# Kernel tuning notes

Hardware: AMD Instinct MI355X
Metric: run time of the kernel (lower is better)

The kernel has to match this reference:

```python
import jax, jax.numpy as jnp
import numpy as np

N_NODES = 50000
N_EDGES = 1600000
LORA_R = 8


def gcn_conv(h, W, b, src, dst, n):
    # PyG GCNConv: linear transform, add self-loops, symmetric normalization,
    # scatter-add aggregation at target nodes, then bias.
    h = h @ W  # [N, out]
    ones = jnp.ones(src.shape[0], dtype=h.dtype)
    deg = jax.ops.segment_sum(ones, dst, num_segments=n) + 1.0  # +1 for self-loop
    dis = jax.lax.rsqrt(deg)  # deg >= 1 always
    norm = dis[src] * dis[dst]  # [E]
    agg = jax.ops.segment_sum(norm[:, None] * h[src], dst, num_segments=n)
    agg = agg + (dis * dis)[:, None] * h  # self-loop contribution
    return agg + b


def lora(h, A, B):
    # LoRALinear: b(a(x)) * (1/r); replaces input (not additive)
    return (h @ A) @ B * (1.0 / LORA_R)


def setup_inputs() -> dict:
    key = jax.random.key(0)
    ks = jax.random.split(key, 12)
    inp = {}
    inp['x'] = jax.random.normal(ks[0], (N_NODES, 128), dtype=jnp.float32)
    inp['edge_index'] = jax.random.randint(ks[1], (2, N_EDGES), 0, N_NODES, dtype=jnp.int64 if jax.config.jax_enable_x64 else jnp.int32)
    inp['domain_idx'] = jax.random.randint(ks[2], (N_NODES,), 0, 3, dtype=jnp.int32)
    inp['emb_table'] = jax.random.normal(ks[3], (3, 4096), dtype=jnp.float32)
    s1 = 1.0 / np.sqrt(4224.0)
    inp['W1'] = jax.random.normal(ks[4], (4224, 32), dtype=jnp.float32) * s1
    inp['b1'] = jnp.zeros((32,), dtype=jnp.float32)
    inp['A1'] = jax.random.normal(ks[5], (32, LORA_R), dtype=jnp.float32) * (1.0 / np.sqrt(32.0))
    inp['B1'] = jax.random.normal(ks[6], (LORA_R, 32), dtype=jnp.float32) * (1.0 / np.sqrt(LORA_R))
    inp['W2'] = jax.random.normal(ks[7], (32, 5), dtype=jnp.float32) * (1.0 / np.sqrt(32.0))
    inp['b2'] = jnp.zeros((5,), dtype=jnp.float32)
    inp['A2'] = jax.random.normal(ks[8], (5, LORA_R), dtype=jnp.float32) * (1.0 / np.sqrt(5.0))
    inp['B2'] = jax.random.normal(ks[9], (LORA_R, 5), dtype=jnp.float32) * (1.0 / np.sqrt(LORA_R))
    return inp


def reference(x, edge_index, domain_idx, emb_table, W1, b1, A1, B1, W2, b2, A2, B2):
    n = x.shape[0]
    src, dst = edge_index[0], edge_index[1]
    embedded = emb_table[domain_idx]  # [N, 4096]
    h = jnp.concatenate([embedded, x], axis=1)  # [N, 4224]
    h = gcn_conv(h, W1, b1, src, dst, n)
    h = lora(h, A1, B1)
    h = jax.nn.relu(h)
    h = gcn_conv(h, W2, b2, src, dst, n)
    h = lora(h, A2, B2)
    return jax.nn.log_softmax(h, axis=1)
```

## Files before the change

### kernel.cpp

```cpp
#include <hip/hip_runtime.h>
#include <hip/hip_bf16.h>
#include <hip/hip_fp16.h>


#define XDIM 128
#define EMBDIM 4096
#define TB 8192
#define BSH 6
#define BN 64
#define ECAP2 2560
#define MAXT 256

__global__ void __launch_bounds__(512) kA(
    const int* __restrict__ src, const int* __restrict__ dst,
    unsigned int* __restrict__ tedges, unsigned int* __restrict__ toffcnt,
    int e, int ntiles,
    const float* __restrict__ emb, const float* __restrict__ W1,
    float* __restrict__ emb_part,
    const float* __restrict__ A1, const float* __restrict__ A2,
    const float* __restrict__ B2, const float* __restrict__ b1,
    float* __restrict__ M2, float* __restrict__ b1A1,
    float* __restrict__ WA, int n) {
    __shared__ __align__(16) char smem[40960];
    int t = threadIdx.x, bx = blockIdx.x;
    if (bx < ntiles) {
        unsigned int* staged = (unsigned int*)smem;
        int* loff = (int*)(smem + 32768);
        int* rctr = (int*)(smem + 36864);
        int base = bx * TB;
        int len = min(TB, e - base);
        for (int i = t; i < 1024; i += 512) { loff[i] = 0; rctr[i] = 0; }
        __syncthreads();
        int sreg[16], dreg[16];
        #pragma unroll
        for (int k = 0; k < 16; ++k) {
            int i = t + k * 512;
            if (i < len) {
                sreg[k] = src[base + i];
                dreg[k] = dst[base + i];
            }
        }
        #pragma unroll
        for (int k = 0; k < 16; ++k) {
            int i = t + k * 512;
            if (i < len) atomicAdd(&loff[dreg[k] >> BSH], 1);
        }
        __syncthreads();
        if (t < 64) {
            int ch = t * 16;
            int v[16]; int s0 = 0;
            #pragma unroll
            for (int k = 0; k < 16; ++k) { v[k] = loff[ch + k]; s0 += v[k]; }
            int pre = s0;
            #pragma unroll
            for (int d2 = 1; d2 < 64; d2 <<= 1) {
                int up = __shfl_up(pre, d2);
                if (t >= d2) pre += up;
            }
            int excl = pre - s0;
            unsigned int* ocp = toffcnt + (size_t)bx * 1024 + ch;
            #pragma unroll
            for (int k = 0; k < 16; ++k) {
                loff[ch + k] = excl;
                ocp[k] = ((unsigned int)excl << 16) | (unsigned int)v[k];
                excl += v[k];
            }
        }
        __syncthreads();
        #pragma unroll
        for (int k = 0; k < 16; ++k) {
            int i = t + k * 512;
            if (i < len) {
                int b = dreg[k] >> BSH;
                int r = atomicAdd(&rctr[b], 1);
                staged[loff[b] + r] = ((unsigned int)dreg[k] << 16) | (unsigned int)sreg[k];
            }
        }
        __syncthreads();
        uint4* tw = (uint4*)(tedges + (size_t)bx * TB);
        const uint4* sr = (const uint4*)staged;
        int lw = (len + 3) >> 2;
        for (int i = t; i < lw; i += 512) tw[i] = sr[i];
    } else if (bx < ntiles + 96) {
        float* red = (float*)smem;
        int bx2 = bx - ntiles;
        int dm = bx2 >> 5, seg = bx2 & 31;
        const float* er = emb + dm * EMBDIM + seg * 128;
        const float* wr = W1 + (size_t)(seg * 128) * 32;
        int j = t & 31, kk = t >> 5;
        if (t < 256) {
            float acc = 0.f;
            for (int k2 = kk; k2 < 128; k2 += 8) acc += er[k2] * wr[k2 * 32 + j];
            red[kk * 32 + j] = acc;
        }
        __syncthreads();
        if (t < 32) {
            float s = 0.f;
            #pragma unroll
            for (int r = 0; r < 8; ++r) s += red[r * 32 + t];
            emb_part[bx2 * 32 + t] = s;
        }
        if (bx2 == 0) {
            if (t < 25) {
                int c = t / 5, cp = t % 5;
                float s = 0.f;
                #pragma unroll
                for (int r = 0; r < 8; ++r) s += A2[c * 8 + r] * B2[r * 5 + cp];
                M2[c * 5 + cp] = s * 0.125f;
            }
            if (t >= 32 && t < 40) {
                int j2 = t - 32;
                float s = 0.f;
                #pragma unroll
                for (int k = 0; k < 32; ++k) s += b1[k] * A1[k * 8 + j2];
                b1A1[j2] = s;
            }
        }
    } else {
        float* sA1 = (float*)smem;
        if (t < 256) sA1[t] = A1[t];
        __syncthreads();
        for (int idx = t; idx < 1024; idx += 512) {
            int k = idx >> 3, j = idx & 7;
            const float* wr = W1 + (size_t)(EMBDIM + k) * 32;
            float s = 0.f;
            #pragma unroll 8
            for (int c = 0; c < 32; ++c) s += wr[c] * sA1[c * 8 + j];
            WA[idx] = s;
        }
    }
}

__global__ void __launch_bounds__(256) kB(
    const unsigned int* __restrict__ tedges, const unsigned int* __restrict__ toffcnt,
    int ntiles,
    const float* __restrict__ emb_part, const float* __restrict__ A1,
    const int* __restrict__ dom, const float* __restrict__ x,
    const float* __restrict__ WA,
    int* __restrict__ deg, __half* __restrict__ p1h,
    unsigned short* __restrict__ nsrc, unsigned int* __restrict__ bm, int n) {
    __shared__ int hist[64], eoff[64], rctr[64], sdom[64];
    __shared__ int wtot[4];
    __shared__ unsigned short rbase[MAXT], soff[MAXT], slen[MAXT];
    __shared__ float sA1[256], sWA[1024], sproj[96], sembA1[24];
    __shared__ __align__(16) unsigned int ebuf[ECAP2];
    __shared__ __align__(16) unsigned short esrc[ECAP2];
    int t = threadIdx.x, b = blockIdx.x;
    int row0 = b << BSH;
    if (t < 64) {
        hist[t] = 0; rctr[t] = 0;
        int gi = row0 + t;
        sdom[t] = (gi < n) ? dom[gi] : 0;
    }
    sA1[t] = A1[t];
    #pragma unroll
    for (int q = 0; q < 4; ++q) sWA[t + q * 256] = WA[t + q * 256];
    if (t < 96) {
        int dm = t >> 5, c = t & 31;
        float s = 0.f;
        #pragma unroll
        for (int seg = 0; seg < 32; ++seg) s += emb_part[(dm * 32 + seg) * 32 + c];
        sproj[dm * 32 + c] = s;
    }
    {
        int w = t >> 6, l = t & 63;
        int i0 = w * 128 + l, i1 = w * 128 + 64 + l;
        unsigned int oc0 = (i0 < ntiles) ? toffcnt[(size_t)i0 * 1024 + b] : 0u;
        unsigned int oc1 = (i1 < ntiles) ? toffcnt[(size_t)i1 * 1024 + b] : 0u;
        int l0 = (int)(oc0 & 0xffffu), l1 = (int)(oc1 & 0xffffu);
        int p0 = l0, p1 = l1;
        #pragma unroll
        for (int d2 = 1; d2 < 64; d2 <<= 1) {
            int u0 = __shfl_up(p0, d2);
            int u1 = __shfl_up(p1, d2);
            if (l >= d2) { p0 += u0; p1 += u1; }
        }
        int totA = __shfl(p0, 63);
        if (l == 63) wtot[w] = p0 + p1;
        __syncthreads();
        int woff = 0;
        #pragma unroll
        for (int q = 0; q < 4; ++q) woff += (q < w) ? wtot[q] : 0;
        if (i0 < ntiles) {
            rbase[i0] = (unsigned short)min(woff + p0 - l0, 65535);
            soff[i0]  = (unsigned short)(oc0 >> 16);
            slen[i0]  = (unsigned short)l0;
        }
        if (i1 < ntiles) {
            rbase[i1] = (unsigned short)min(woff + totA + p1 - l1, 65535);
            soff[i1]  = (unsigned short)(oc1 >> 16);
            slen[i1]  = (unsigned short)l1;
        }
        if (t == 0) wtot[0] = wtot[0] + wtot[1] + wtot[2] + wtot[3];
    }
    __syncthreads();
    int m = wtot[0];
    if (m > ECAP2) m = ECAP2;
    if (t == 0) bm[b] = (unsigned int)m;
    {
        int g4 = t >> 2, l4 = t & 3;
        for (int tl = g4; tl < ntiles; tl += 64) {
            int l = slen[tl];
            if (l > 0) {
                const unsigned int* rp = tedges + (size_t)tl * TB + soff[tl];
                int bse = rbase[tl];
                for (int j = l4; j < l; j += 4) {
                    int p = bse + j;
                    if (p < ECAP2) ebuf[p] = rp[j];
                }
            }
        }
    }
    __syncthreads();
    for (int i = t; i < m; i += 256) atomicAdd(&hist[(ebuf[i] >> 16) & (BN - 1)], 1);
    __syncthreads();
    if (t < 64) {
        int v = hist[t];
        int pre = v;
        #pragma unroll
        for (int d2 = 1; d2 < 64; d2 <<= 1) {
            int up = __shfl_up(pre, d2);
            if (t >= d2) pre += up;
        }
        eoff[t] = pre - v;
        int gi = row0 + t;
        if (gi < n) deg[gi] = v;
    } else if (t < 88) {
        int dm = (t - 64) >> 3, j = (t - 64) & 7;
        float s = 0.f;
        #pragma unroll 8
        for (int c = 0; c < 32; ++c) s += sproj[dm * 32 + c] * sA1[c * 8 + j];
        sembA1[dm * 8 + j] = s;
    }
    __syncthreads();
    for (int i = t; i < m; i += 256) {
        unsigned int u = ebuf[i];
        int dl = (int)(u >> 16) & (BN - 1);
        int r = atomicAdd(&rctr[dl], 1);
        esrc[eoff[dl] + r] = (unsigned short)(u & 0xffffu);
    }
    for (int i = t; i < 512; i += 256) {
        int row = i >> 3, j = i & 7;
        int gi = row0 + row;
        if (gi < n) {
            const float4* xr = (const float4*)x + (size_t)gi * 32;
            float acc = 0.f;
            #pragma unroll 8
            for (int c4 = 0; c4 < 32; ++c4) {
                float4 v = xr[c4];
                acc += v.x * sWA[(c4 * 4 + 0) * 8 + j]
                     + v.y * sWA[(c4 * 4 + 1) * 8 + j]
                     + v.z * sWA[(c4 * 4 + 2) * 8 + j]
                     + v.w * sWA[(c4 * 4 + 3) * 8 + j];
            }
            float dd = rsqrtf((float)(hist[row] + 1));
            float val = acc + sembA1[sdom[row] * 8 + j];
            p1h[(size_t)gi * 8 + j] = __float2half_rn(dd * val);
        }
    }
    __syncthreads();
    {
        uint4* npw = (uint4*)(nsrc + (size_t)b * ECAP2);
        const uint4* ew = (const uint4*)esrc;
        int mw = (m + 7) >> 3;
        for (int i = t; i < mw; i += 256) npw[i] = ew[i];
    }
}

__global__ void __launch_bounds__(256) k_bagg1(
    const __half* __restrict__ p1h, const unsigned short* __restrict__ nsrc,
    const unsigned int* __restrict__ bm, const int* __restrict__ deg,
    const float* __restrict__ b1A1, const float* __restrict__ B1,
    const float* __restrict__ W2, __half* __restrict__ qh, int n) {
    __shared__ __align__(16) unsigned short esrc[ECAP2];
    __shared__ int eoff[BN], sdeg[BN];
    __shared__ float pacc[3][BN][8];
    __shared__ float sB1[256], sW2[160], sb[8];
    int t = threadIdx.x, b = blockIdx.x;
    int node0 = b << BSH;
    sB1[t] = B1[t];
    if (t < 160) sW2[t] = W2[t];
    if (t < 8) sb[t] = b1A1[t];
    if (t < 64) {
        int node = node0 + t;
        int v = (node < n) ? deg[node] : 0;
        sdeg[t] = v;
        int pre = v;
        #pragma unroll
        for (int d2 = 1; d2 < 64; d2 <<= 1) {
            int up = __shfl_up(pre, d2);
            if (t >= d2) pre += up;
        }
        eoff[t] = pre - v;
    }
    __syncthreads();
    int m = (int)bm[b];
    if (m > ECAP2) m = ECAP2;
    {
        const uint4* npw = (const uint4*)(nsrc + (size_t)b * ECAP2);
        uint4* ew = (uint4*)esrc;
        int mw = (m + 7) >> 3;
        for (int i = t; i < mw; i += 256) ew[i] = npw[i];
    }
    __syncthreads();
    int nodeL = t & (BN - 1), tsub = t >> BSH;
    int base0 = eoff[nodeL], c = sdeg[nodeL];
    float a[8] = {0,0,0,0,0,0,0,0}, a2[8] = {0,0,0,0,0,0,0,0};
    float a3[8] = {0,0,0,0,0,0,0,0}, a4[8] = {0,0,0,0,0,0,0,0};
    int k = tsub;
    for (; k + 12 < c; k += 16) {
        int s1 = esrc[base0 + k],     s2 = esrc[base0 + k + 4];
        int s3 = esrc[base0 + k + 8], s4 = esrc[base0 + k + 12];
        uint4 u = *(const uint4*)(p1h + (size_t)s1 * 8);
        uint4 v = *(const uint4*)(p1h + (size_t)s2 * 8);
        uint4 w = *(const uint4*)(p1h + (size_t)s3 * 8);
        uint4 y = *(const uint4*)(p1h + (size_t)s4 * 8);
        float2 f;
        f = __half22float2(*(__half2*)&u.x); a[0] += f.x; a[1] += f.y;
        f = __half22float2(*(__half2*)&u.y); a[2] += f.x; a[3] += f.y;
        f = __half22float2(*(__half2*)&u.z); a[4] += f.x; a[5] += f.y;
        f = __half22float2(*(__half2*)&u.w); a[6] += f.x; a[7] += f.y;
        f = __half22float2(*(__half2*)&v.x); a2[0] += f.x; a2[1] += f.y;
        f = __half22float2(*(__half2*)&v.y); a2[2] += f.x; a2[3] += f.y;
        f = __half22float2(*(__half2*)&v.z); a2[4] += f.x; a2[5] += f.y;
        f = __half22float2(*(__half2*)&v.w); a2[6] += f.x; a2[7] += f.y;
        f = __half22float2(*(__half2*)&w.x); a3[0] += f.x; a3[1] += f.y;
        f = __half22float2(*(__half2*)&w.y); a3[2] += f.x; a3[3] += f.y;
        f = __half22float2(*(__half2*)&w.z); a3[4] += f.x; a3[5] += f.y;
        f = __half22float2(*(__half2*)&w.w); a3[6] += f.x; a3[7] += f.y;
        f = __half22float2(*(__half2*)&y.x); a4[0] += f.x; a4[1] += f.y;
        f = __half22float2(*(__half2*)&y.y); a4[2] += f.x; a4[3] += f.y;
        f = __half22float2(*(__half2*)&y.z); a4[4] += f.x; a4[5] += f.y;
        f = __half22float2(*(__half2*)&y.w); a4[6] += f.x; a4[7] += f.y;
    }
    for (; k + 4 < c; k += 8) {
        int s1 = esrc[base0 + k], s2 = esrc[base0 + k + 4];
        uint4 u = *(const uint4*)(p1h + (size_t)s1 * 8);
        uint4 v = *(const uint4*)(p1h + (size_t)s2 * 8);
        float2 f;
        f = __half22float2(*(__half2*)&u.x); a[0] += f.x; a[1] += f.y;
        f = __half22float2(*(__half2*)&u.y); a[2] += f.x; a[3] += f.y;
        f = __half22float2(*(__half2*)&u.z); a[4] += f.x; a[5] += f.y;
        f = __half22float2(*(__half2*)&u.w); a[6] += f.x; a[7] += f.y;
        f = __half22float2(*(__half2*)&v.x); a2[0] += f.x; a2[1] += f.y;
        f = __half22float2(*(__half2*)&v.y); a2[2] += f.x; a2[3] += f.y;
        f = __half22float2(*(__half2*)&v.z); a2[4] += f.x; a2[5] += f.y;
        f = __half22float2(*(__half2*)&v.w); a2[6] += f.x; a2[7] += f.y;
    }
    for (; k < c; k += 4) {
        int s1 = esrc[base0 + k];
        uint4 u = *(const uint4*)(p1h + (size_t)s1 * 8);
        float2 f;
        f = __half22float2(*(__half2*)&u.x); a[0] += f.x; a[1] += f.y;
        f = __half22float2(*(__half2*)&u.y); a[2] += f.x; a[3] += f.y;
        f = __half22float2(*(__half2*)&u.z); a[4] += f.x; a[5] += f.y;
        f = __half22float2(*(__half2*)&u.w); a[6] += f.x; a[7] += f.y;
    }
    #pragma unroll
    for (int j = 0; j < 8; ++j) a[j] += a2[j] + a3[j] + a4[j];
    if (tsub > 0) {
        #pragma unroll
        for (int j = 0; j < 8; ++j) pacc[tsub - 1][nodeL][j] = a[j];
    }
    __syncthreads();
    if (t < BN) {
        int node = node0 + t;
        if (node < n) {
            float dd = rsqrtf((float)(sdeg[t] + 1));
            uint4 u = *(const uint4*)(p1h + (size_t)node * 8);
            float2 f;
            float af[8];
            f = __half22float2(*(__half2*)&u.x); af[0] = a[0] + f.x; af[1] = a[1] + f.y;
            f = __half22float2(*(__half2*)&u.y); af[2] = a[2] + f.x; af[3] = a[3] + f.y;
            f = __half22float2(*(__half2*)&u.z); af[4] = a[4] + f.x; af[5] = a[5] + f.y;
            f = __half22float2(*(__half2*)&u.w); af[6] = a[6] + f.x; af[7] = a[7] + f.y;
            #pragma unroll
            for (int ps = 0; ps < 3; ++ps) {
                #pragma unroll
                for (int j = 0; j < 8; ++j) af[j] += pacc[ps][t][j];
            }
            #pragma unroll
            for (int j = 0; j < 8; ++j) af[j] = dd * af[j] + sb[j];
            float qv[5] = {0.f, 0.f, 0.f, 0.f, 0.f};
            #pragma unroll
            for (int c2 = 0; c2 < 32; ++c2) {
                float tv = 0.f;
                #pragma unroll
                for (int j = 0; j < 8; ++j) tv += af[j] * sB1[j * 32 + c2];
                float st = fmaxf(tv * 0.125f, 0.f);
                #pragma unroll
                for (int o = 0; o < 5; ++o) qv[o] += st * sW2[c2 * 5 + o];
            }
            #pragma unroll
            for (int o = 0; o < 5; ++o) qh[(size_t)node * 8 + o] = __float2half_rn(dd * qv[o]);
        }
    }
}

__global__ void __launch_bounds__(256) k_bagg2(
    const __half* __restrict__ qh, const unsigned short* __restrict__ nsrc,
    const unsigned int* __restrict__ bm, const int* __restrict__ deg,
    const float* __restrict__ b2, const float* __restrict__ M2,
    float* __restrict__ out, int n) {
    __shared__ __align__(16) unsigned short esrc[ECAP2];
    __shared__ int eoff[BN], sdeg[BN];
    __shared__ float pacc[3][BN][5];
    __shared__ float sM2[25], sb2[5];
    int t = threadIdx.x, b = blockIdx.x;
    int node0 = b << BSH;
    if (t < 25) sM2[t] = M2[t];
    if (t < 5) sb2[t] = b2[t];
    if (t < 64) {
        int node = node0 + t;
        int v = (node < n) ? deg[node] : 0;
        sdeg[t] = v;
        int pre = v;
        #pragma unroll
        for (int d2 = 1; d2 < 64; d2 <<= 1) {
            int up = __shfl_up(pre, d2);
            if (t >= d2) pre += up;
        }
        eoff[t] = pre - v;
    }
    __syncthreads();
    int m = (int)bm[b];
    if (m > ECAP2) m = ECAP2;
    {
        const uint4* npw = (const uint4*)(nsrc + (size_t)b * ECAP2);
        uint4* ew = (uint4*)esrc;
        int mw = (m + 7) >> 3;
        for (int i = t; i < mw; i += 256) ew[i] = npw[i];
    }
    __syncthreads();
    int nodeL = t & (BN - 1), tsub = t >> BSH;
    int base0 = eoff[nodeL], c = sdeg[nodeL];
    float a[5] = {0,0,0,0,0}, a2[5] = {0,0,0,0,0};
    float a3[5] = {0,0,0,0,0}, a4[5] = {0,0,0,0,0};
    int k = tsub;
    for (; k + 12 < c; k += 16) {
        int s1 = esrc[base0 + k],     s2 = esrc[base0 + k + 4];
        int s3 = esrc[base0 + k + 8], s4 = esrc[base0 + k + 12];
        uint4 u = *(const uint4*)(qh + (size_t)s1 * 8);
        uint4 v = *(const uint4*)(qh + (size_t)s2 * 8);
        uint4 w = *(const uint4*)(qh + (size_t)s3 * 8);
        uint4 y = *(const uint4*)(qh + (size_t)s4 * 8);
        float2 f;
        f = __half22float2(*(__half2*)&u.x); a[0] += f.x; a[1] += f.y;
        f = __half22float2(*(__half2*)&u.y); a[2] += f.x; a[3] += f.y;
        f = __half22float2(*(__half2*)&u.z); a[4] += f.x;
        f = __half22float2(*(__half2*)&v.x); a2[0] += f.x; a2[1] += f.y;
        f = __half22float2(*(__half2*)&v.y); a2[2] += f.x; a2[3] += f.y;
        f = __half22float2(*(__half2*)&v.z); a2[4] += f.x;
        f = __half22float2(*(__half2*)&w.x); a3[0] += f.x; a3[1] += f.y;
        f = __half22float2(*(__half2*)&w.y); a3[2] += f.x; a3[3] += f.y;
        f = __half22float2(*(__half2*)&w.z); a3[4] += f.x;
        f = __half22float2(*(__half2*)&y.x); a4[0] += f.x; a4[1] += f.y;
        f = __half22float2(*(__half2*)&y.y); a4[2] += f.x; a4[3] += f.y;
        f = __half22float2(*(__half2*)&y.z); a4[4] += f.x;
    }
    for (; k + 4 < c; k += 8) {
        int s1 = esrc[base0 + k], s2 = esrc[base0 + k + 4];
        uint4 u = *(const uint4*)(qh + (size_t)s1 * 8);
        uint4 v = *(const uint4*)(qh + (size_t)s2 * 8);
        float2 f;
        f = __half22float2(*(__half2*)&u.x); a[0] += f.x; a[1] += f.y;
        f = __half22float2(*(__half2*)&u.y); a[2] += f.x; a[3] += f.y;
        f = __half22float2(*(__half2*)&u.z); a[4] += f.x;
        f = __half22float2(*(__half2*)&v.x); a2[0] += f.x; a2[1] += f.y;
        f = __half22float2(*(__half2*)&v.y); a2[2] += f.x; a2[3] += f.y;
        f = __half22float2(*(__half2*)&v.z); a2[4] += f.x;
    }
    for (; k < c; k += 4) {
        int s1 = esrc[base0 + k];
        uint4 u = *(const uint4*)(qh + (size_t)s1 * 8);
        float2 f;
        f = __half22float2(*(__half2*)&u.x); a[0] += f.x; a[1] += f.y;
        f = __half22float2(*(__half2*)&u.y); a[2] += f.x; a[3] += f.y;
        f = __half22float2(*(__half2*)&u.z); a[4] += f.x;
    }
    #pragma unroll
    for (int j = 0; j < 5; ++j) a[j] += a2[j] + a3[j] + a4[j];
    if (tsub > 0) {
        #pragma unroll
        for (int j = 0; j < 5; ++j) pacc[tsub - 1][nodeL][j] = a[j];
    }
    __syncthreads();
    if (t < BN) {
        int node = node0 + t;
        if (node < n) {
            float dd = rsqrtf((float)(sdeg[t] + 1));
            uint4 u = *(const uint4*)(qh + (size_t)node * 8);
            float2 f;
            float av[5];
            f = __half22float2(*(__half2*)&u.x); av[0] = a[0] + f.x; av[1] = a[1] + f.y;
            f = __half22float2(*(__half2*)&u.y); av[2] = a[2] + f.x; av[3] = a[3] + f.y;
            f = __half22float2(*(__half2*)&u.z); av[4] = a[4] + f.x;
            #pragma unroll
            for (int ps = 0; ps < 3; ++ps) {
                #pragma unroll
                for (int j = 0; j < 5; ++j) av[j] += pacc[ps][t][j];
            }
            #pragma unroll
            for (int j = 0; j < 5; ++j) av[j] = dd * av[j] + sb2[j];
            float z[5];
            #pragma unroll
            for (int cp = 0; cp < 5; ++cp) {
                float s = 0.f;
                #pragma unroll
                for (int c2 = 0; c2 < 5; ++c2) s += av[c2] * sM2[c2 * 5 + cp];
                z[cp] = s;
            }
            float mx = z[0];
            #pragma unroll
            for (int c2 = 1; c2 < 5; ++c2) mx = fmaxf(mx, z[c2]);
            float ssum = 0.f;
            #pragma unroll
            for (int c2 = 0; c2 < 5; ++c2) ssum += __expf(z[c2] - mx);
            float ls = __logf(ssum);
            #pragma unroll
            for (int c2 = 0; c2 < 5; ++c2) out[node * 5 + c2] = z[c2] - mx - ls;
        }
    }
}

extern "C" void kernel_launch(void* const* d_in, const int* in_sizes, int n_in,
                              void* d_out, int out_size, void* d_ws, size_t ws_size,
                              hipStream_t stream) {
    const float* x   = (const float*)d_in[0];
    const int*   ei  = (const int*)d_in[1];
    const int*   dom = (const int*)d_in[2];
    const float* emb = (const float*)d_in[3];
    const float* W1  = (const float*)d_in[4];
    const float* b1  = (const float*)d_in[5];
    const float* A1  = (const float*)d_in[6];
    const float* B1  = (const float*)d_in[7];
    const float* W2  = (const float*)d_in[8];
    const float* b2  = (const float*)d_in[9];
    const float* A2  = (const float*)d_in[10];
    const float* B2  = (const float*)d_in[11];
    float* out = (float*)d_out;

    int n = in_sizes[2];
    int e = in_sizes[1] / 2;
    const int* src = ei;
    const int* dst = ei + e;

    int ntiles = (e + TB - 1) / TB;
    int nbuck  = (n + BN - 1) >> BSH;

    char* base = (char*)d_ws;
    size_t o = 0;
    auto carve = [&](size_t bytes) {
        void* p = base + o;
        o = (o + bytes + 15) & ~(size_t)15;
        return p;
    };
    float* emb_part = (float*)carve(96 * 32 * sizeof(float));
    float* M2       = (float*)carve(32 * sizeof(float));
    float* b1A1     = (float*)carve(8 * sizeof(float));
    float* WA       = (float*)carve(1024 * sizeof(float));
    unsigned int* bm = (unsigned int*)carve(1024 * sizeof(int));
    int*   deg      = (int*)carve((size_t)n * sizeof(int));
    __half* p1h     = (__half*)carve((size_t)n * 8 * sizeof(__half));
    __half* qh      = (__half*)carve((size_t)n * 8 * sizeof(__half));
    unsigned int* tedges  = (unsigned int*)carve((size_t)ntiles * TB * sizeof(unsigned int));
    unsigned int* toffcnt = (unsigned int*)carve((size_t)ntiles * 1024 * sizeof(unsigned int));
    unsigned short* nsrc  = (unsigned short*)carve((size_t)nbuck * ECAP2 * sizeof(unsigned short));
    (void)ws_size; (void)n_in; (void)out_size;

    kA<<<ntiles + 97, 512, 0, stream>>>(
        src, dst, tedges, toffcnt, e, ntiles,
        emb, W1, emb_part, A1, A2, B2, b1, M2, b1A1, WA, n);
    kB<<<nbuck, 256, 0, stream>>>(tedges, toffcnt, ntiles, emb_part, A1, dom,
                                  x, WA, deg, p1h, nsrc, bm, n);
    k_bagg1<<<nbuck, 256, 0, stream>>>(p1h, nsrc, bm, deg, b1A1, B1, W2, qh, n);
    k_bagg2<<<nbuck, 256, 0, stream>>>(qh, nsrc, bm, deg, b2, M2, out, n);
}
```

Before: 143.4 us.

## Double node bucket size to 128 rows per block with two threads per node

Raises the per-block node bucket from 64 to 128 nodes and the edge capacity accordingly, halving the number of blocks in the bucketing and aggregation kernels. Each node is now served by two threads instead of four, so the prefix scans handle two values per lane and the partial-sum reduction shrinks to one buffer. Fewer blocks cut the per-block scan of tile offsets and redundant per-block setup, at the cost of less parallelism per node, more shared memory per block, and a larger chance of overflowing the edge capacity. Launch grid sizes and the partitioning in kA must also be consistent with the new bucket size, and they are not shown.

```diff
diff --git a/kernel.cpp b/kernel.cpp
--- a/kernel.cpp
+++ b/kernel.cpp
@@ -6,9 +6,9 @@
 #define XDIM 128
 #define EMBDIM 4096
 #define TB 8192
-#define BSH 6
-#define BN 64
-#define ECAP2 2560
+#define BSH 7
+#define BN 128
+#define ECAP2 4736
 #define MAXT 256
 
 __global__ void __launch_bounds__(512) kA(
@@ -139,7 +139,7 @@
     const float* __restrict__ WA,
     int* __restrict__ deg, __half* __restrict__ p1h,
     unsigned short* __restrict__ nsrc, unsigned int* __restrict__ bm, int n) {
-    __shared__ int hist[64], eoff[64], rctr[64], sdom[64];
+    __shared__ int hist[BN], eoff[BN], rctr[BN], sdom[BN];
     __shared__ int wtot[4];
     __shared__ unsigned short rbase[MAXT], soff[MAXT], slen[MAXT];
     __shared__ float sA1[256], sWA[1024], sproj[96], sembA1[24];
@@ -147,7 +147,7 @@
     __shared__ __align__(16) unsigned short esrc[ECAP2];
     int t = threadIdx.x, b = blockIdx.x;
     int row0 = b << BSH;
-    if (t < 64) {
+    if (t < BN) {
         hist[t] = 0; rctr[t] = 0;
         int gi = row0 + t;
         sdom[t] = (gi < n) ? dom[gi] : 0;
@@ -198,13 +198,13 @@
     if (m > ECAP2) m = ECAP2;
     if (t == 0) bm[b] = (unsigned int)m;
     {
-        int g4 = t >> 2, l4 = t & 3;
-        for (int tl = g4; tl < ntiles; tl += 64) {
+        int g8 = t >> 3, l8 = t & 7;
+        for (int tl = g8; tl < ntiles; tl += 32) {
             int l = slen[tl];
             if (l > 0) {
                 const unsigned int* rp = tedges + (size_t)tl * TB + soff[tl];
                 int bse = rbase[tl];
-                for (int j = l4; j < l; j += 4) {
+                for (int j = l8; j < l; j += 8) {
                     int p = bse + j;
                     if (p < ECAP2) ebuf[p] = rp[j];
                 }
@@ -215,16 +215,20 @@
     for (int i = t; i < m; i += 256) atomicAdd(&hist[(ebuf[i] >> 16) & (BN - 1)], 1);
     __syncthreads();
     if (t < 64) {
-        int v = hist[t];
-        int pre = v;
+        int v0 = hist[t], v1 = hist[t + 64];
+        int p0 = v0, p1 = v1;
         #pragma unroll
         for (int d2 = 1; d2 < 64; d2 <<= 1) {
-            int up = __shfl_up(pre, d2);
-            if (t >= d2) pre += up;
-        }
-        eoff[t] = pre - v;
-        int gi = row0 + t;
-        if (gi < n) deg[gi] = v;
+            int u0 = __shfl_up(p0, d2);
+            int u1 = __shfl_up(p1, d2);
+            if (t >= d2) { p0 += u0; p1 += u1; }
+        }
+        int tot0 = __shfl(p0, 63);
+        eoff[t] = p0 - v0;
+        eoff[t + 64] = tot0 + p1 - v1;
+        int g0 = row0 + t, g1 = row0 + t + 64;
+        if (g0 < n) deg[g0] = v0;
+        if (g1 < n) deg[g1] = v1;
     } else if (t < 88) {
         int dm = (t - 64) >> 3, j = (t - 64) & 7;
         float s = 0.f;
@@ -239,7 +243,7 @@
         int r = atomicAdd(&rctr[dl], 1);
         esrc[eoff[dl] + r] = (unsigned short)(u & 0xffffu);
     }
-    for (int i = t; i < 512; i += 256) {
+    for (int i = t; i < BN * 8; i += 256) {
         int row = i >> 3, j = i & 7;
         int gi = row0 + row;
         if (gi < n) {
@@ -274,7 +278,7 @@
     const float* __restrict__ W2, __half* __restrict__ qh, int n) {
     __shared__ __align__(16) unsigned short esrc[ECAP2];
     __shared__ int eoff[BN], sdeg[BN];
-    __shared__ float pacc[3][BN][8];
+    __shared__ float pacc[1][BN][8];
     __shared__ float sB1[256], sW2[160], sb[8];
     int t = threadIdx.x, b = blockIdx.x;
     int node0 = b << BSH;
@@ -282,16 +286,20 @@
     if (t < 160) sW2[t] = W2[t];
     if (t < 8) sb[t] = b1A1[t];
     if (t < 64) {
-        int node = node0 + t;
-        int v = (node < n) ? deg[node] : 0;
-        sdeg[t] = v;
-        int pre = v;
+        int n0 = node0 + t, n1 = node0 + t + 64;
+        int v0 = (n0 < n) ? deg[n0] : 0;
+        int v1 = (n1 < n) ? deg[n1] : 0;
+        sdeg[t] = v0; sdeg[t + 64] = v1;
+        int p0 = v0, p1 = v1;
         #pragma unroll
         for (int d2 = 1; d2 < 64; d2 <<= 1) {
-            int up = __shfl_up(pre, d2);
-            if (t >= d2) pre += up;
-        }
-        eoff[t] = pre - v;
+            int u0 = __shfl_up(p0, d2);
+            int u1 = __shfl_up(p1, d2);
+            if (t >= d2) { p0 += u0; p1 += u1; }
+        }
+        int tot0 = __shfl(p0, 63);
+        eoff[t] = p0 - v0;
+        eoff[t + 64] = tot0 + p1 - v1;
     }
     __syncthreads();
     int m = (int)bm[b];
@@ -308,9 +316,9 @@
     float a[8] = {0,0,0,0,0,0,0,0}, a2[8] = {0,0,0,0,0,0,0,0};
     float a3[8] = {0,0,0,0,0,0,0,0}, a4[8] = {0,0,0,0,0,0,0,0};
     int k = tsub;
-    for (; k + 12 < c; k += 16) {
-        int s1 = esrc[base0 + k],     s2 = esrc[base0 + k + 4];
-        int s3 = esrc[base0 + k + 8], s4 = esrc[base0 + k + 12];
+    for (; k + 6 < c; k += 8) {
+        int s1 = esrc[base0 + k],     s2 = esrc[base0 + k + 2];
+        int s3 = esrc[base0 + k + 4], s4 = esrc[base0 + k + 6];
         uint4 u = *(const uint4*)(p1h + (size_t)s1 * 8);
         uint4 v = *(const uint4*)(p1h + (size_t)s2 * 8);
         uint4 w = *(const uint4*)(p1h + (size_t)s3 * 8);
@@ -333,21 +341,7 @@
         f = __half22float2(*(__half2*)&y.z); a4[4] += f.x; a4[5] += f.y;
         f = __half22float2(*(__half2*)&y.w); a4[6] += f.x; a4[7] += f.y;
     }
-    for (; k + 4 < c; k += 8) {
-        int s1 = esrc[base0 + k], s2 = esrc[base0 + k + 4];
-        uint4 u = *(const uint4*)(p1h + (size_t)s1 * 8);
-        uint4 v = *(const uint4*)(p1h + (size_t)s2 * 8);
-        float2 f;
-        f = __half22float2(*(__half2*)&u.x); a[0] += f.x; a[1] += f.y;
-        f = __half22float2(*(__half2*)&u.y); a[2] += f.x; a[3] += f.y;
-        f = __half22float2(*(__half2*)&u.z); a[4] += f.x; a[5] += f.y;
-        f = __half22float2(*(__half2*)&u.w); a[6] += f.x; a[7] += f.y;
-        f = __half22float2(*(__half2*)&v.x); a2[0] += f.x; a2[1] += f.y;
-        f = __half22float2(*(__half2*)&v.y); a2[2] += f.x; a2[3] += f.y;
-        f = __half22float2(*(__half2*)&v.z); a2[4] += f.x; a2[5] += f.y;
-        f = __half22float2(*(__half2*)&v.w); a2[6] += f.x; a2[7] += f.y;
-    }
-    for (; k < c; k += 4) {
+    for (; k < c; k += 2) {
         int s1 = esrc[base0 + k];
         uint4 u = *(const uint4*)(p1h + (size_t)s1 * 8);
         float2 f;
@@ -360,7 +354,7 @@
     for (int j = 0; j < 8; ++j) a[j] += a2[j] + a3[j] + a4[j];
     if (tsub > 0) {
         #pragma unroll
-        for (int j = 0; j < 8; ++j) pacc[tsub - 1][nodeL][j] = a[j];
+        for (int j = 0; j < 8; ++j) pacc[0][nodeL][j] = a[j];
     }
     __syncthreads();
     if (t < BN) {
@@ -375,10 +369,7 @@
             f = __half22float2(*(__half2*)&u.z); af[4] = a[4] + f.x; af[5] = a[5] + f.y;
             f = __half22float2(*(__half2*)&u.w); af[6] = a[6] + f.x; af[7] = a[7] + f.y;
             #pragma unroll
-            for (int ps = 0; ps < 3; ++ps) {
-                #pragma unroll
-                for (int j = 0; j < 8; ++j) af[j] += pacc[ps][t][j];
-            }
+            for (int j = 0; j < 8; ++j) af[j] += pacc[0][t][j];
             #pragma unroll
             for (int j = 0; j < 8; ++j) af[j] = dd * af[j] + sb[j];
             float qv[5] = {0.f, 0.f, 0.f, 0.f, 0.f};
@@ -404,23 +395,27 @@
     float* __restrict__ out, int n) {
     __shared__ __align__(16) unsigned short esrc[ECAP2];
     __shared__ int eoff[BN], sdeg[BN];
-    __shared__ float pacc[3][BN][5];
+    __shared__ float pacc[1][BN][5];
     __shared__ float sM2[25], sb2[5];
     int t = threadIdx.x, b = blockIdx.x;
     int node0 = b << BSH;
     if (t < 25) sM2[t] = M2[t];
     if (t < 5) sb2[t] = b2[t];
     if (t < 64) {
-        int node = node0 + t;
-        int v = (node < n) ? deg[node] : 0;
-        sdeg[t] = v;
-        int pre = v;
+        int n0 = node0 + t, n1 = node0 + t + 64;
+        int v0 = (n0 < n) ? deg[n0] : 0;
+        int v1 = (n1 < n) ? deg[n1] : 0;
+        sdeg[t] = v0; sdeg[t + 64] = v1;
+        int p0 = v0, p1 = v1;
         #pragma unroll
         for (int d2 = 1; d2 < 64; d2 <<= 1) {
-            int up = __shfl_up(pre, d2);
-            if (t >= d2) pre += up;
-        }
-        eoff[t] = pre - v;
+            int u0 = __shfl_up(p0, d2);
+            int u1 = __shfl_up(p1, d2);
+            if (t >= d2) { p0 += u0; p1 += u1; }
+        }
+        int tot0 = __shfl(p0, 63);
+        eoff[t] = p0 - v0;
+        eoff[t + 64] = tot0 + p1 - v1;
     }
     __syncthreads();
     int m = (int)bm[b];
@@ -437,9 +432,9 @@
     float a[5] = {0,0,0,0,0}, a2[5] = {0,0,0,0,0};
     float a3[5] = {0,0,0,0,0}, a4[5] = {0,0,0,0,0};
     int k = tsub;
-    for (; k + 12 < c; k += 16) {
-        int s1 = esrc[base0 + k],     s2 = esrc[base0 + k + 4];
-        int s3 = esrc[base0 + k + 8], s4 = esrc[base0 + k + 12];
+    for (; k + 6 < c; k += 8) {
+        int s1 = esrc[base0 + k],     s2 = esrc[base0 + k + 2];
+        int s3 = esrc[base0 + k + 4], s4 = esrc[base0 + k + 6];
         uint4 u = *(const uint4*)(qh + (size_t)s1 * 8);
         uint4 v = *(const uint4*)(qh + (size_t)s2 * 8);
         uint4 w = *(const uint4*)(qh + (size_t)s3 * 8);
@@ -458,19 +453,7 @@
         f = __half22float2(*(__half2*)&y.y); a4[2] += f.x; a4[3] += f.y;
         f = __half22float2(*(__half2*)&y.z); a4[4] += f.x;
     }
-    for (; k + 4 < c; k += 8) {
-        int s1 = esrc[base0 + k], s2 = esrc[base0 + k + 4];
-        uint4 u = *(const uint4*)(qh + (size_t)s1 * 8);
-        uint4 v = *(const uint4*)(qh + (size_t)s2 * 8);
-        float2 f;
-        f = __half22float2(*(__half2*)&u.x); a[0] += f.x; a[1] += f.y;
-        f = __half22float2(*(__half2*)&u.y); a[2] += f.x; a[3] += f.y;
-        f = __half22float2(*(__half2*)&u.z); a[4] += f.x;
-        f = __half22float2(*(__half2*)&v.x); a2[0] += f.x; a2[1] += f.y;
-        f = __half22float2(*(__half2*)&v.y); a2[2] += f.x; a2[3] += f.y;
-        f = __half22float2(*(__half2*)&v.z); a2[4] += f.x;
-    }
-    for (; k < c; k += 4) {
+    for (; k < c; k += 2) {
         int s1 = esrc[base0 + k];
         uint4 u = *(const uint4*)(qh + (size_t)s1 * 8);
         float2 f;
@@ -482,7 +465,7 @@
     for (int j = 0; j < 5; ++j) a[j] += a2[j] + a3[j] + a4[j];
     if (tsub > 0) {
         #pragma unroll
-        for (int j = 0; j < 5; ++j) pacc[tsub - 1][nodeL][j] = a[j];
+        for (int j = 0; j < 5; ++j) pacc[0][nodeL][j] = a[j];
     }
     __syncthreads();
     if (t < BN) {
@@ -496,10 +479,7 @@
             f = __half22float2(*(__half2*)&u.y); av[2] = a[2] + f.x; av[3] = a[3] + f.y;
             f = __half22float2(*(__half2*)&u.z); av[4] = a[4] + f.x;
             #pragma unroll
-            for (int ps = 0; ps < 3; ++ps) {
-                #pragma unroll
-                for (int j = 0; j < 5; ++j) av[j] += pacc[ps][t][j];
-            }
+            for (int j = 0; j < 5; ++j) av[j] += pacc[0][t][j];
             #pragma unroll
             for (int j = 0; j < 5; ++j) av[j] = dd * av[j] + sb2[j];
             float z[5];
```

Measured after the change: 149.1 us. 4.0% more time.
